# Optimization experiments

Hardware: AMD Instinct MI355X
Metric: run time of the kernel (lower is better)

## Reference

```python
import jax, jax.numpy as jnp
import numpy as np

N_NODES = 50000
N_EDGES = 800000
IN_DIM = 128
HID_DIM = 64


def gcn_conv(x, W, b, src, dst, ew):
    """PyG GCNConv with edge_weight: add self-loops (weight 1), symmetric
    normalization D^-1/2 (A+I) D^-1/2, linear transform, scatter-add, bias."""
    n = x.shape[0]
    loop = jnp.arange(n)
    src_a = jnp.concatenate([src, loop])           # [E+N]
    dst_a = jnp.concatenate([dst, loop])
    ew_a = jnp.concatenate([ew, jnp.ones((n,), dtype=x.dtype)])
    deg = jax.ops.segment_sum(ew_a, dst_a, num_segments=n)   # [N]
    dinv = jnp.where(deg > 0, jax.lax.rsqrt(deg), 0.0)
    norm = dinv[src_a] * ew_a * dinv[dst_a]        # [E+N]
    h = x @ W                                      # [N, out]
    msg = h[src_a] * norm[:, None]                 # gather + scale
    out = jax.ops.segment_sum(msg, dst_a, num_segments=n)    # scatter-add
    return out + b


def setup_inputs() -> dict:
    key = jax.random.key(0)
    k = jax.random.split(key, 6)
    x = jax.random.normal(k[0], (N_NODES, IN_DIM), dtype=jnp.float32)
    edge_index = jax.random.randint(k[1], (2, N_EDGES), 0, N_NODES, dtype=jnp.int64)
    edge_weight = jax.random.uniform(k[2], (N_EDGES,), dtype=jnp.float32)
    W1 = jax.random.normal(k[3], (IN_DIM, HID_DIM), dtype=jnp.float32) * (1.0 / np.sqrt(IN_DIM))
    b1 = jnp.zeros((HID_DIM,), dtype=jnp.float32)
    W2 = jax.random.normal(k[4], (HID_DIM, 1), dtype=jnp.float32) * (1.0 / np.sqrt(HID_DIM))
    b2 = jnp.zeros((1,), dtype=jnp.float32)
    return {"x": x, "edge_index": edge_index, "edge_weight": edge_weight,
            "W1": W1, "b1": b1, "W2": W2, "b2": b2}


def reference(x, edge_index, edge_weight, W1, b1, W2, b2):
    src, dst = edge_index[0], edge_index[1]
    h = gcn_conv(x, W1, b1, src, dst, edge_weight)
    h = jax.nn.relu(h)
    h = gcn_conv(h, W2, b2, src, dst, edge_weight)
    return jax.nn.sigmoid(h).squeeze(-1)           # [N]
```

## Files before the change

### kernel.cpp

```cpp
#include <hip/hip_runtime.h>
#include <hip/hip_bf16.h>
#include <math.h>

#define N_NODES 50000
#define N_EDGES 800000
#define IN_DIM  128
#define HID_DIM 64

#define NBKT     196
#define BKT_CAP  5000
#define NPASSC   200
#define EDGES_PER_PASSC (N_EDGES / NPASSC)
#define NGEMM    3125

__global__ __launch_bounds__(256)
void partgemm_kernel(const int* __restrict__ src, const int* __restrict__ dst,
                     const float* __restrict__ ew, int* __restrict__ gcursor,
                     int2* __restrict__ edge_b,
                     const float* __restrict__ x, const float* __restrict__ W1,
                     __hip_bfloat16* __restrict__ h1b) {
    __shared__ float w1s[IN_DIM * HID_DIM];
    int bid = blockIdx.x;
    int tid = threadIdx.x;
    if (bid < NPASSC) {
        int* cnt1    = (int*)w1s;
        int* cnt2    = cnt1 + NBKT;
        int* runbase = cnt2 + NBKT;
        if (tid < NBKT) { cnt1[tid] = 0; cnt2[tid] = 0; }
        __syncthreads();
        int e0 = bid * EDGES_PER_PASSC;
        for (int i = tid; i < EDGES_PER_PASSC; i += 256)
            atomicAdd(&cnt1[dst[e0 + i] >> 8], 1);
        __syncthreads();
        if (tid < NBKT) {
            int c = cnt1[tid];
            runbase[tid] = (c > 0) ? atomicAdd(&gcursor[tid], c) : 0;
        }
        __syncthreads();
        for (int i = tid; i < EDGES_PER_PASSC; i += 256) {
            int e = e0 + i;
            int d = dst[e];
            int b = d >> 8;
            int lr = atomicAdd(&cnt2[b], 1);
            int pos = b * BKT_CAP + runbase[b] + lr;
            edge_b[pos] = make_int2(src[e] | ((d & 255) << 16), __float_as_int(ew[e]));
        }
        return;
    }
    int gb = bid - NPASSC;
    int wv   = tid >> 6;
    int lane = tid & 63;
    int node0 = gb * 16;
    const float4* W4 = (const float4*)W1;
    float4* w1s4 = (float4*)w1s;
#pragma unroll
    for (int i = 0; i < 8; ++i) w1s4[tid + 256 * i] = W4[tid + 256 * i];
    __syncthreads();
    int k0 = __builtin_amdgcn_readfirstlane(wv) * 32;
    float Wreg[32];
#pragma unroll
    for (int kk = 0; kk < 32; ++kk) Wreg[kk] = w1s[(k0 + kk) * HID_DIM + lane];
    __syncthreads();
    float* psum = w1s;
    const float* xbase = x + (long)node0 * IN_DIM + k0;
#pragma unroll
    for (int n = 0; n < 16; n += 2) {
        const float4* xa4 = (const float4*)(xbase + (long)n * IN_DIM);
        const float4* xb4 = (const float4*)(xbase + (long)(n + 1) * IN_DIM);
        float accA = 0.f, accB = 0.f;
#pragma unroll
        for (int q = 0; q < 8; ++q) {
            float4 xa = xa4[q];
            float4 xb = xb4[q];
            accA += xa.x * Wreg[4*q+0] + xa.y * Wreg[4*q+1] + xa.z * Wreg[4*q+2] + xa.w * Wreg[4*q+3];
            accB += xb.x * Wreg[4*q+0] + xb.y * Wreg[4*q+1] + xb.z * Wreg[4*q+2] + xb.w * Wreg[4*q+3];
        }
        psum[(wv * 16 + n) * 64 + lane]     = accA;
        psum[(wv * 16 + n + 1) * 64 + lane] = accB;
    }
    __syncthreads();
#pragma unroll
    for (int i = 0; i < 4; ++i) {
        int n = wv * 4 + i;
        float s = psum[n * 64 + lane] + psum[(16 + n) * 64 + lane]
                + psum[(32 + n) * 64 + lane] + psum[(48 + n) * 64 + lane];
        h1b[(long)(node0 + n) * HID_DIM + lane] = __float2bfloat16(s);
    }
}

__global__ __launch_bounds__(1024)
void bsort_kernel(const int* __restrict__ gcursor, const int2* __restrict__ edge_b,
                  int2* __restrict__ edge_s, int* __restrict__ start_g,
                  int* __restrict__ cnt_g, float* __restrict__ dinv) {
    __shared__ int   cnt[256];
    __shared__ int   cnt2[256];
    __shared__ float deg[256];
    __shared__ int   sc[256];
    int b   = blockIdx.x;
    int tid = threadIdx.x;
    int M    = gcursor[b];
    int base = b * BKT_CAP;
    if (tid < 256) { cnt[tid] = 0; cnt2[tid] = 0; deg[tid] = 0.0f; }
    __syncthreads();
    for (int i = tid; i < M; i += 1024) {
        int2 e = edge_b[base + i];
        int ld = (e.x >> 16) & 255;
        atomicAdd(&cnt[ld], 1);
        atomicAdd(&deg[ld], __int_as_float(e.y));
    }
    __syncthreads();
    if (tid < 256) sc[tid] = cnt[tid];
    __syncthreads();
#pragma unroll
    for (int off = 1; off < 256; off <<= 1) {
        int t = (tid >= off && tid < 256) ? sc[tid - off] : 0;
        __syncthreads();
        if (tid < 256) sc[tid] += t;
        __syncthreads();
    }
    if (tid < 256) {
        int startL = sc[tid] - cnt[tid];
        int node = b * 256 + tid;
        if (node < N_NODES) {
            start_g[node] = base + startL;
            cnt_g[node]   = cnt[tid];
            dinv[node]    = rsqrtf(1.0f + deg[tid]);
        }
        sc[tid] = startL;
    }
    __syncthreads();
    for (int i = tid; i < M; i += 1024) {
        int2 e = edge_b[base + i];
        int ld = (e.x >> 16) & 255;
        int r = atomicAdd(&cnt2[ld], 1);
        edge_s[base + sc[ld] + r] = make_int2(e.x & 0xFFFF, e.y);
    }
}

__global__ void gather1_layer2_kernel(const int* __restrict__ start_g, const int* __restrict__ cnt_g,
                                      const int2* __restrict__ edge_s,
                                      const __hip_bfloat16* __restrict__ h1b,
                                      const float* __restrict__ dinv, const float* __restrict__ b1,
                                      const float* __restrict__ W2, float* __restrict__ h2s) {
    __shared__ int2 meta[4][64];
    int wave = (blockIdx.x * blockDim.x + threadIdx.x) >> 6;
    int wl = threadIdx.x >> 6;
    int lane = threadIdx.x & 63;
    if (wave >= N_NODES) return;
    int s0 = start_g[wave];
    int ctotal = cnt_g[wave];
    int c0 = (lane & 31) * 2;
    int half = lane >> 5;
    float accA = 0.f, accB = 0.f;
    float accA2 = 0.f, accB2 = 0.f;
    for (int done = 0; done < ctotal; done += 64) {
        int cnt = ctotal - done;
        if (cnt > 64) cnt = 64;
        if (lane < cnt) {
            int2 m = edge_s[s0 + done + lane];
            float w = __int_as_float(m.y) * dinv[m.x];
            meta[wl][lane] = make_int2(m.x, __float_as_int(w));
        }
        __builtin_amdgcn_wave_barrier();
        int cnte = cnt & ~1;
        int j = 0;
        for (; j + 16 <= cnte; j += 16) {
            int2 m0 = meta[wl][j +  0 + half];
            int2 m1 = meta[wl][j +  2 + half];
            int2 m2 = meta[wl][j +  4 + half];
            int2 m3 = meta[wl][j +  6 + half];
            int2 m4 = meta[wl][j +  8 + half];
            int2 m5 = meta[wl][j + 10 + half];
            int2 m6 = meta[wl][j + 12 + half];
            int2 m7 = meta[wl][j + 14 + half];
            unsigned int p0 = *(const unsigned int*)&h1b[m0.x * HID_DIM + c0];
            unsigned int p1 = *(const unsigned int*)&h1b[m1.x * HID_DIM + c0];
            unsigned int p2 = *(const unsigned int*)&h1b[m2.x * HID_DIM + c0];
            unsigned int p3 = *(const unsigned int*)&h1b[m3.x * HID_DIM + c0];
            unsigned int p4 = *(const unsigned int*)&h1b[m4.x * HID_DIM + c0];
            unsigned int p5 = *(const unsigned int*)&h1b[m5.x * HID_DIM + c0];
            unsigned int p6 = *(const unsigned int*)&h1b[m6.x * HID_DIM + c0];
            unsigned int p7 = *(const unsigned int*)&h1b[m7.x * HID_DIM + c0];
            float w0 = __int_as_float(m0.y), w1 = __int_as_float(m1.y);
            float w2 = __int_as_float(m2.y), w3 = __int_as_float(m3.y);
            float w4 = __int_as_float(m4.y), w5 = __int_as_float(m5.y);
            float w6 = __int_as_float(m6.y), w7 = __int_as_float(m7.y);
            accA  += w0 * __uint_as_float(p0 << 16);
            accB  += w0 * __uint_as_float(p0 & 0xFFFF0000u);
            accA2 += w1 * __uint_as_float(p1 << 16);
            accB2 += w1 * __uint_as_float(p1 & 0xFFFF0000u);
            accA  += w2 * __uint_as_float(p2 << 16);
            accB  += w2 * __uint_as_float(p2 & 0xFFFF0000u);
            accA2 += w3 * __uint_as_float(p3 << 16);
            accB2 += w3 * __uint_as_float(p3 & 0xFFFF0000u);
            accA  += w4 * __uint_as_float(p4 << 16);
            accB  += w4 * __uint_as_float(p4 & 0xFFFF0000u);
            accA2 += w5 * __uint_as_float(p5 << 16);
            accB2 += w5 * __uint_as_float(p5 & 0xFFFF0000u);
            accA  += w6 * __uint_as_float(p6 << 16);
            accB  += w6 * __uint_as_float(p6 & 0xFFFF0000u);
            accA2 += w7 * __uint_as_float(p7 << 16);
            accB2 += w7 * __uint_as_float(p7 & 0xFFFF0000u);
        }
        for (; j + 2 <= cnte; j += 2) {
            int2 m = meta[wl][j + half];
            unsigned int p = *(const unsigned int*)&h1b[m.x * HID_DIM + c0];
            accA += __int_as_float(m.y) * __uint_as_float(p << 16);
            accB += __int_as_float(m.y) * __uint_as_float(p & 0xFFFF0000u);
        }
        if (cnt & 1) {
            if (half == 0) {
                int2 m = meta[wl][cnt - 1];
                unsigned int p = *(const unsigned int*)&h1b[m.x * HID_DIM + c0];
                accA += __int_as_float(m.y) * __uint_as_float(p << 16);
                accB += __int_as_float(m.y) * __uint_as_float(p & 0xFFFF0000u);
            }
        }
        __builtin_amdgcn_wave_barrier();
    }
    accA += accA2; accB += accB2;
    accA += __shfl_xor(accA, 32, 64);
    accB += __shfl_xor(accB, 32, 64);
    float di = dinv[wave];
    unsigned int sp = *(const unsigned int*)&h1b[wave * HID_DIM + c0];
    float s0f = __uint_as_float(sp << 16);
    float s1f = __uint_as_float(sp & 0xFFFF0000u);
    float z0 = di * (accA + di * s0f) + b1[c0];
    float z1 = di * (accB + di * s1f) + b1[c0 + 1];
    float h0 = fmaxf(z0, 0.0f);
    float h1v = fmaxf(z1, 0.0f);
    float v = h0 * W2[c0] + h1v * W2[c0 + 1];
#pragma unroll
    for (int off = 16; off > 0; off >>= 1)
        v += __shfl_down(v, off, 32);
    if (lane == 0) h2s[wave] = v * di;
}

__global__ void gather2_final_kernel(const int* __restrict__ start_g, const int* __restrict__ cnt_g,
                                     const int2* __restrict__ edge_s,
                                     const float* __restrict__ h2s, const float* __restrict__ dinv,
                                     const float* __restrict__ b2, float* __restrict__ out) {
    int t = blockIdx.x * blockDim.x + threadIdx.x;
    int n = t >> 4;
    int sub = t & 15;
    if (n >= N_NODES) return;
    int s0 = start_g[n];
    int cnt = cnt_g[n];
    float acc = 0.0f;
    for (int j = sub; j < cnt; j += 16) {
        int2 m = edge_s[s0 + j];
        acc += __int_as_float(m.y) * h2s[m.x];
    }
#pragma unroll
    for (int off = 8; off > 0; off >>= 1)
        acc += __shfl_down(acc, off, 16);
    if (sub == 0) {
        float z = dinv[n] * (acc + h2s[n]) + b2[0];
        out[n] = 1.0f / (1.0f + expf(-z));
    }
}

extern "C" void kernel_launch(void* const* d_in, const int* in_sizes, int n_in,
                              void* d_out, int out_size, void* d_ws, size_t ws_size,
                              hipStream_t stream) {
    const float* x  = (const float*)d_in[0];
    const int*   ei = (const int*)d_in[1];
    const float* ew = (const float*)d_in[2];
    const float* W1 = (const float*)d_in[3];
    const float* b1 = (const float*)d_in[4];
    const float* W2 = (const float*)d_in[5];
    const float* b2 = (const float*)d_in[6];
    float* out = (float*)d_out;

    const int* src = ei;
    const int* dst = ei + N_EDGES;

    char* ws = (char*)d_ws;
    int2*  edge_b  = (int2*)ws;              ws += (size_t)NBKT * BKT_CAP * sizeof(int2);
    int2*  edge_s  = (int2*)ws;              ws += (size_t)NBKT * BKT_CAP * sizeof(int2);
    int*   gcursor = (int*)ws;               ws += NBKT * sizeof(int);
    int*   start_g = (int*)ws;               ws += N_NODES * sizeof(int);
    int*   cnt_g   = (int*)ws;               ws += N_NODES * sizeof(int);
    float* dinv    = (float*)ws;             ws += N_NODES * sizeof(float);
    float* h2s     = (float*)ws;             ws += N_NODES * sizeof(float);
    ws = (char*)(((uintptr_t)ws + 127) & ~(uintptr_t)127);
    __hip_bfloat16* h1b = (__hip_bfloat16*)ws;

    hipMemsetAsync(gcursor, 0, NBKT * sizeof(int), stream);
    partgemm_kernel<<<NPASSC + NGEMM, 256, 0, stream>>>(src, dst, ew, gcursor, edge_b, x, W1, h1b);
    bsort_kernel<<<NBKT, 1024, 0, stream>>>(gcursor, edge_b, edge_s, start_g, cnt_g, dinv);
    gather1_layer2_kernel<<<(N_NODES * 64) / 256, 256, 0, stream>>>(start_g, cnt_g, edge_s, h1b, dinv, b1, W2, h2s);
    gather2_final_kernel<<<(N_NODES * 16 + 255) / 256, 256, 0, stream>>>(start_g, cnt_g, edge_s, h2s, dinv, b2, out);
}
```

Before: 163.2 us.

## Tile GEMM block with 64 nodes staged in shared memory and 4x4 register blocking

Rewrites the GEMM part of the fused partition/GEMM kernel. Each block now handles 64 nodes instead of 16 and stages their x rows in padded shared memory. Each thread computes a 4x4 output tile from shared-memory W and x, which removes the split-K partial-sum reduction and raises reuse of W per block load. The cost is more LDS per block (about 32KB plus 33KB), which may lower occupancy, and a grid of 782 blocks with tail guards for the final partial tile.

```diff
diff --git a/kernel.cpp b/kernel.cpp
--- a/kernel.cpp
+++ b/kernel.cpp
@@ -11,7 +11,9 @@
 #define BKT_CAP  5000
 #define NPASSC   200
 #define EDGES_PER_PASSC (N_EDGES / NPASSC)
-#define NGEMM    3125
+#define GEMM_NODES 64
+#define NGEMM    782
+#define XS_LD    132
 
 __global__ __launch_bounds__(256)
 void partgemm_kernel(const int* __restrict__ src, const int* __restrict__ dst,
@@ -20,6 +22,7 @@
                      const float* __restrict__ x, const float* __restrict__ W1,
                      __hip_bfloat16* __restrict__ h1b) {
     __shared__ float w1s[IN_DIM * HID_DIM];
+    __shared__ float xs[GEMM_NODES][XS_LD];
     int bid = blockIdx.x;
     int tid = threadIdx.x;
     if (bid < NPASSC) {
@@ -48,43 +51,53 @@
         return;
     }
     int gb = bid - NPASSC;
-    int wv   = tid >> 6;
-    int lane = tid & 63;
-    int node0 = gb * 16;
+    int node0 = gb * GEMM_NODES;
     const float4* W4 = (const float4*)W1;
     float4* w1s4 = (float4*)w1s;
 #pragma unroll
     for (int i = 0; i < 8; ++i) w1s4[tid + 256 * i] = W4[tid + 256 * i];
-    __syncthreads();
-    int k0 = __builtin_amdgcn_readfirstlane(wv) * 32;
-    float Wreg[32];
-#pragma unroll
-    for (int kk = 0; kk < 32; ++kk) Wreg[kk] = w1s[(k0 + kk) * HID_DIM + lane];
-    __syncthreads();
-    float* psum = w1s;
-    const float* xbase = x + (long)node0 * IN_DIM + k0;
-#pragma unroll
-    for (int n = 0; n < 16; n += 2) {
-        const float4* xa4 = (const float4*)(xbase + (long)n * IN_DIM);
-        const float4* xb4 = (const float4*)(xbase + (long)(n + 1) * IN_DIM);
-        float accA = 0.f, accB = 0.f;
-#pragma unroll
-        for (int q = 0; q < 8; ++q) {
-            float4 xa = xa4[q];
-            float4 xb = xb4[q];
-            accA += xa.x * Wreg[4*q+0] + xa.y * Wreg[4*q+1] + xa.z * Wreg[4*q+2] + xa.w * Wreg[4*q+3];
-            accB += xb.x * Wreg[4*q+0] + xb.y * Wreg[4*q+1] + xb.z * Wreg[4*q+2] + xb.w * Wreg[4*q+3];
-        }
-        psum[(wv * 16 + n) * 64 + lane]     = accA;
-        psum[(wv * 16 + n + 1) * 64 + lane] = accB;
-    }
-    __syncthreads();
+    {
+        int r = tid >> 2, q = tid & 3;
+        int row = node0 + r;
+        if (row >= N_NODES) row = N_NODES - 1;
+        const float4* xr = (const float4*)(x + (long)row * IN_DIM + q * 32);
+#pragma unroll
+        for (int i = 0; i < 8; ++i)
+            *(float4*)&xs[r][q * 32 + i * 4] = xr[i];
+    }
+    __syncthreads();
+    int w    = tid >> 6;
+    int lane = tid & 63;
+    int ng   = lane >> 2;
+    int jg   = lane & 3;
+    int j0   = w * 16 + jg * 4;
+    float acc[4][4] = {{0.f}};
+#pragma unroll 2
+    for (int k = 0; k < IN_DIM; k += 4) {
+        float4 wr0 = *(const float4*)&w1s[(k + 0) * HID_DIM + j0];
+        float4 wr1 = *(const float4*)&w1s[(k + 1) * HID_DIM + j0];
+        float4 wr2 = *(const float4*)&w1s[(k + 2) * HID_DIM + j0];
+        float4 wr3 = *(const float4*)&w1s[(k + 3) * HID_DIM + j0];
+#pragma unroll
+        for (int i = 0; i < 4; ++i) {
+            float4 xv = *(const float4*)&xs[ng + 16 * i][k];
+            acc[i][0] += xv.x * wr0.x + xv.y * wr1.x + xv.z * wr2.x + xv.w * wr3.x;
+            acc[i][1] += xv.x * wr0.y + xv.y * wr1.y + xv.z * wr2.y + xv.w * wr3.y;
+            acc[i][2] += xv.x * wr0.z + xv.y * wr1.z + xv.z * wr2.z + xv.w * wr3.z;
+            acc[i][3] += xv.x * wr0.w + xv.y * wr1.w + xv.z * wr2.w + xv.w * wr3.w;
+        }
+    }
 #pragma unroll
     for (int i = 0; i < 4; ++i) {
-        int n = wv * 4 + i;
-        float s = psum[n * 64 + lane] + psum[(16 + n) * 64 + lane]
-                + psum[(32 + n) * 64 + lane] + psum[(48 + n) * 64 + lane];
-        h1b[(long)(node0 + n) * HID_DIM + lane] = __float2bfloat16(s);
+        int n = node0 + ng + 16 * i;
+        if (n < N_NODES) {
+            __hip_bfloat16 bf[4];
+            bf[0] = __float2bfloat16(acc[i][0]);
+            bf[1] = __float2bfloat16(acc[i][1]);
+            bf[2] = __float2bfloat16(acc[i][2]);
+            bf[3] = __float2bfloat16(acc[i][3]);
+            *(uint2*)&h1b[(long)n * HID_DIM + j0] = *(uint2*)bf;
+        }
     }
 }
 
```

After: 155.1 us. 1.05x faster.
